# Performance work log

Measured on AMD Instinct MI355X. Metric: run time of the kernel, lower is better.

## Reference

```python
import jax, jax.numpy as jnp
import numpy as np

B, S, L, T = 32, 512, 20, 16
E, H, D = 300, 128, 128
V = 50000
SEG = S // T


def _gru_dir(x, Wi, Wh, bi, bh, reverse):
    """One direction of torch-style GRU. x: (B,S,E). Returns (outs (B,S,H), h_final (B,H))."""
    xs = jnp.swapaxes(x, 0, 1)  # (S,B,E)
    h0 = jnp.zeros((x.shape[0], H), x.dtype)

    def step(h, x_t):
        gi = x_t @ Wi.T + bi          # (B,3H) gates order: r,z,n (torch)
        gh = h @ Wh.T + bh
        r = jax.nn.sigmoid(gi[:, :H] + gh[:, :H])
        z = jax.nn.sigmoid(gi[:, H:2 * H] + gh[:, H:2 * H])
        n = jnp.tanh(gi[:, 2 * H:] + r * gh[:, 2 * H:])
        h_new = (1.0 - z) * n + z * h
        return h_new, h_new

    hN, hs = jax.lax.scan(step, h0, xs, reverse=reverse)
    return jnp.swapaxes(hs, 0, 1), hN


def setup_inputs() -> dict:
    key = jax.random.key(0)
    ks = jax.random.split(key, 16)
    word_ids = jax.random.randint(ks[0], (B, S, L), 0, V, dtype=jnp.int32)
    # contiguous, full-coverage topic segments, 1-based boundaries (as in the torch code)
    starts = jnp.tile(jnp.arange(T, dtype=jnp.int32) * SEG + 1, (B, 1))
    ends = jnp.tile((jnp.arange(T, dtype=jnp.int32) + 1) * SEG, (B, 1))
    sent2topic = jnp.tile((jnp.arange(S, dtype=jnp.int32) // SEG), (B, 1))
    sc = 0.08
    return {
        "word_ids": word_ids, "starts": starts, "ends": ends, "sent2topic": sent2topic,
        "embed_table": jax.random.normal(ks[1], (V, E), jnp.float32) * 0.6,
        "Wi_f": jax.random.normal(ks[2], (3 * H, E), jnp.float32) * sc,
        "Wh_f": jax.random.normal(ks[3], (3 * H, H), jnp.float32) * sc,
        "bi_f": jax.random.normal(ks[4], (3 * H,), jnp.float32) * sc,
        "bh_f": jax.random.normal(ks[5], (3 * H,), jnp.float32) * sc,
        "Wi_b": jax.random.normal(ks[6], (3 * H, E), jnp.float32) * sc,
        "Wh_b": jax.random.normal(ks[7], (3 * H, H), jnp.float32) * sc,
        "bi_b": jax.random.normal(ks[8], (3 * H,), jnp.float32) * sc,
        "bh_b": jax.random.normal(ks[9], (3 * H,), jnp.float32) * sc,
        "W_att": jax.random.normal(ks[10], (4 * H, 4 * H), jnp.float32) * 0.05,
        "v_att": jax.random.normal(ks[11], (4 * H, 1), jnp.float32) * 0.05,
        "W1": jax.random.normal(ks[12], (D, 4 * H), jnp.float32) * 0.05,
        "b1": jax.random.normal(ks[13], (D,), jnp.float32) * 0.05,
        "W2": jax.random.normal(ks[14], (1, D), jnp.float32) * 0.05,
        "b2": jax.random.normal(ks[15], (1,), jnp.float32) * 0.05,
    }


def reference(word_ids, starts, ends, sent2topic, embed_table,
              Wi_f, Wh_f, bi_f, bh_f, Wi_b, Wh_b, bi_b, bh_b,
              W_att, v_att, W1, b1, W2, b2):
    # --- sent_encoder: mean of word embeddings per sentence ---
    sent = jnp.take(embed_table, word_ids, axis=0).mean(axis=2)  # (B,S,E)
    # --- doc_encoder: bidirectional GRU ---
    out_f, h_f = _gru_dir(sent, Wi_f, Wh_f, bi_f, bh_f, reverse=False)
    out_b, h_b = _gru_dir(sent, Wi_b, Wh_b, bi_b, bh_b, reverse=True)
    sent_rep = jnp.concatenate([out_f, out_b], axis=-1)          # (B,S,2H)
    # faithful to torch: hidden (2,B,H).view(B,2H)
    hidden = jnp.stack([h_f, h_b], axis=0)
    doc_rep = hidden.reshape(B, 2 * H)
    doc_rep = jnp.broadcast_to(doc_rep[None], (S, B, 2 * H)).swapaxes(0, 1)  # (B,S,2H)
    # --- topic_rep: boundary diffs (padded index i == 1-based sentence i) ---
    padded = jnp.pad(sent_rep, ((0, 0), (1, 1), (0, 0)))          # (B,S+2,2H)
    g = lambda idx: jnp.take_along_axis(padded, idx[:, :, None], axis=1)  # (B,T,2H)
    fwd_diff = g(ends)[..., :H] - g(starts - 1)[..., :H]
    bwd_diff = g(starts)[..., H:] - g(ends + 1)[..., H:]
    topic_mat = jnp.concatenate([fwd_diff, bwd_diff], axis=-1)   # (B,T,2H)
    topic_rep = jnp.take_along_axis(topic_mat, sent2topic[:, :, None], axis=1)  # (B,S,2H)
    # --- decoder ---
    cat_ds = jnp.concatenate([doc_rep, sent_rep], axis=-1)       # (B,S,4H)
    cat_ts = jnp.concatenate([topic_rep, sent_rep], axis=-1)
    doc_scores = jnp.tanh(cat_ds @ W_att) @ v_att                # (B,S,1)
    topic_scores = jnp.tanh(cat_ts @ W_att) @ v_att
    sum_scores = doc_scores + topic_scores
    doc_w = doc_scores / sum_scores
    topic_w = topic_scores / sum_scores
    context = doc_w * doc_rep + topic_w * topic_rep
    inp = jnp.concatenate([sent_rep, context], axis=-1)          # (B,S,4H)
    h = jax.nn.relu(inp @ W1.T + b1)                             # dropout=eval identity
    logits = (h @ W2.T + b2).squeeze(-1)                         # (B,S)
    return logits
```

## Files before the change

kernel.cpp:

```cpp
#include <hip/hip_runtime.h>


#define LDS_BARRIER() do {                                   \
    asm volatile("s_waitcnt lgkmcnt(0)" ::: "memory");       \
    __builtin_amdgcn_s_barrier();                            \
    asm volatile("" ::: "memory");                           \
  } while (0)

__global__ __launch_bounds__(128) void k_sent_mean(
    const int* __restrict__ wid, const float* __restrict__ emb,
    float* __restrict__ sent)
{
  const int bs = blockIdx.x;
  const int tid = threadIdx.x;
  const int* w = wid + (size_t)bs * 20;
  float a0 = 0.f, a1 = 0.f, a2 = 0.f;
  for (int l = 0; l < 20; ++l) {
    const float* row = emb + (size_t)w[l] * 300;
    a0 += row[tid];
    a1 += row[tid + 128];
    if (tid < 44) a2 += row[tid + 256];
  }
  const float inv = 1.0f / 20.0f;
  float* o = sent + (size_t)bs * 300;
  o[tid] = a0 * inv;
  o[tid + 128] = a1 * inv;
  if (tid < 44) o[tid + 256] = a2 * inv;
}

template<bool BT, int ACT>
__global__ __launch_bounds__(256) void k_gemm(
    const int M, const int N, const int K,
    const float* __restrict__ A, const int lda,
    const float* __restrict__ Bm, const int ldb,
    float* __restrict__ C, const int ldc,
    const float* __restrict__ bias)
{
  (void)N;
  __shared__ float As[64][68];
  __shared__ float Bs[64][68];
  const int tid = threadIdx.x;
  const int m0 = blockIdx.x * 64;
  const int n0 = blockIdx.y * 64;
  const int tx = tid & 15;
  const int ty = tid >> 4;
  float acc[4][4] = {};

  for (int kc = 0; kc < K; kc += 64) {
    const int kb = (K - kc < 64) ? (K - kc) : 64;
    #pragma unroll
    for (int r = 0; r < 4; ++r) {
      const int m = r * 16 + ty;
      const int k4 = tx * 4;
      float4 v = make_float4(0.f, 0.f, 0.f, 0.f);
      if (m0 + m < M) {
        const float* ap = A + (size_t)(m0 + m) * lda + kc;
        if (k4 + 4 <= kb) {
          v = *(const float4*)(ap + k4);
        } else {
          float t0 = (k4 + 0 < kb) ? ap[k4 + 0] : 0.f;
          float t1 = (k4 + 1 < kb) ? ap[k4 + 1] : 0.f;
          float t2 = (k4 + 2 < kb) ? ap[k4 + 2] : 0.f;
          float t3 = (k4 + 3 < kb) ? ap[k4 + 3] : 0.f;
          v = make_float4(t0, t1, t2, t3);
        }
      }
      *(float4*)&As[m][k4] = v;
    }
    if (BT) {
      #pragma unroll
      for (int r = 0; r < 4; ++r) {
        const int n = r * 16 + ty;
        const int k4 = tx * 4;
        float4 v = make_float4(0.f, 0.f, 0.f, 0.f);
        const float* bp = Bm + (size_t)(n0 + n) * ldb + kc;
        if (k4 + 4 <= kb) {
          v = *(const float4*)(bp + k4);
        } else {
          float t0 = (k4 + 0 < kb) ? bp[k4 + 0] : 0.f;
          float t1 = (k4 + 1 < kb) ? bp[k4 + 1] : 0.f;
          float t2 = (k4 + 2 < kb) ? bp[k4 + 2] : 0.f;
          float t3 = (k4 + 3 < kb) ? bp[k4 + 3] : 0.f;
          v = make_float4(t0, t1, t2, t3);
        }
        Bs[k4 + 0][n] = v.x;
        Bs[k4 + 1][n] = v.y;
        Bs[k4 + 2][n] = v.z;
        Bs[k4 + 3][n] = v.w;
      }
    } else {
      #pragma unroll
      for (int r = 0; r < 4; ++r) {
        const int kk = r * 16 + ty;
        const int n4 = tx * 4;
        float4 v = make_float4(0.f, 0.f, 0.f, 0.f);
        if (kk < kb) v = *(const float4*)(Bm + (size_t)(kc + kk) * ldb + n0 + n4);
        *(float4*)&Bs[kk][n4] = v;
      }
    }
    __syncthreads();
    #pragma unroll 4
    for (int kk = 0; kk < kb; ++kk) {
      const float4 bv = *(const float4*)&Bs[kk][tx * 4];
      #pragma unroll
      for (int i = 0; i < 4; ++i) {
        const float a = As[ty * 4 + i][kk];
        acc[i][0] = fmaf(a, bv.x, acc[i][0]);
        acc[i][1] = fmaf(a, bv.y, acc[i][1]);
        acc[i][2] = fmaf(a, bv.z, acc[i][2]);
        acc[i][3] = fmaf(a, bv.w, acc[i][3]);
      }
    }
    __syncthreads();
  }

  float bv4[4] = {0.f, 0.f, 0.f, 0.f};
  if (bias != nullptr) {
    #pragma unroll
    for (int j = 0; j < 4; ++j) bv4[j] = bias[n0 + tx * 4 + j];
  }
  #pragma unroll
  for (int i = 0; i < 4; ++i) {
    const int m = m0 + ty * 4 + i;
    if (m < M) {
      float4 o;
      o.x = acc[i][0] + bv4[0];
      o.y = acc[i][1] + bv4[1];
      o.z = acc[i][2] + bv4[2];
      o.w = acc[i][3] + bv4[3];
      if (ACT == 1) {
        o.x = fmaxf(o.x, 0.f); o.y = fmaxf(o.y, 0.f);
        o.z = fmaxf(o.z, 0.f); o.w = fmaxf(o.w, 0.f);
      }
      *(float4*)&C[(size_t)m * ldc + n0 + tx * 4] = o;
    }
  }
}

__global__ __launch_bounds__(512, 2) void k_gru(
    const float* __restrict__ gi_f, const float* __restrict__ gi_b,
    const float* __restrict__ Wh_f, const float* __restrict__ Wh_b,
    const float* __restrict__ bh_f, const float* __restrict__ bh_b,
    float* __restrict__ srep, float* __restrict__ hfin)
{
  const int dir = blockIdx.x & 1;
  const int b = blockIdx.x >> 1;
  const float* gi = (dir ? gi_b : gi_f) + (size_t)b * 512 * 384;
  const float* Wh = dir ? Wh_b : Wh_f;
  const float* bh = dir ? bh_b : bh_f;

  const int tid = threadIdx.x;
  const int wv = tid >> 6;
  const int ln = tid & 63;
  const int kq = wv & 3;
  const int rg = wv >> 2;
  const int r0 = rg * 192 + ln;

  __shared__ __align__(16) float hlds[128];
  __shared__ float partl[4 * 384];
  __shared__ __align__(16) float gis[2][32 * 384];

  float4 w0[8], w1[8], w2[8];
  {
    const float* p = Wh + (size_t)r0 * 128 + kq * 32;
    #pragma unroll
    for (int kk = 0; kk < 8; ++kk) w0[kk] = *(const float4*)(p + kk * 4);
    p += 64 * 128;
    #pragma unroll
    for (int kk = 0; kk < 8; ++kk) w1[kk] = *(const float4*)(p + kk * 4);
    p += 64 * 128;
    #pragma unroll
    for (int kk = 0; kk < 8; ++kk) w2[kk] = *(const float4*)(p + kk * 4);
  }
  const float bh0 = (kq == 0) ? bh[r0] : 0.f;
  const float bh1 = (kq == 0) ? bh[r0 + 64] : 0.f;
  const float bh2 = (kq == 0) ? bh[r0 + 128] : 0.f;

  {
    const int lo0 = dir ? 480 : 0;
    const float4* g4 = (const float4*)(gi + (size_t)lo0 * 384);
    float4* l4 = (float4*)gis[0];
    #pragma unroll
    for (int j = 0; j < 6; ++j) l4[j * 512 + tid] = g4[j * 512 + tid];
  }
  float hreg = 0.f;
  if (tid < 128) hlds[tid] = 0.f;
  LDS_BARRIER();

  const float4* h4q = (const float4*)hlds + kq * 8;
  float4 stg[6];

  for (int c = 0; c < 16; ++c) {
    const int buf = c & 1;
    const int lo = dir ? (480 - 32 * c) : (32 * c);
    if (c < 15) {
      const int lon = dir ? (480 - 32 * (c + 1)) : (32 * (c + 1));
      const float4* g4 = (const float4*)(gi + (size_t)lon * 384);
      #pragma unroll
      for (int j = 0; j < 6; ++j) stg[j] = g4[j * 512 + tid];
    }

    for (int i = 0; i < 32; ++i) {
      const int sloc = dir ? (31 - i) : i;
      const int seq = lo + sloc;

      float4 A0 = {0.f, 0.f, 0.f, 0.f};
      float4 A1 = {0.f, 0.f, 0.f, 0.f};
      float4 A2 = {0.f, 0.f, 0.f, 0.f};
      #pragma unroll
      for (int kk = 0; kk < 8; ++kk) {
        const float4 hv = h4q[kk];
        A0.x = fmaf(w0[kk].x, hv.x, A0.x);
        A0.y = fmaf(w0[kk].y, hv.y, A0.y);
        A0.z = fmaf(w0[kk].z, hv.z, A0.z);
        A0.w = fmaf(w0[kk].w, hv.w, A0.w);
        A1.x = fmaf(w1[kk].x, hv.x, A1.x);
        A1.y = fmaf(w1[kk].y, hv.y, A1.y);
        A1.z = fmaf(w1[kk].z, hv.z, A1.z);
        A1.w = fmaf(w1[kk].w, hv.w, A1.w);
        A2.x = fmaf(w2[kk].x, hv.x, A2.x);
        A2.y = fmaf(w2[kk].y, hv.y, A2.y);
        A2.z = fmaf(w2[kk].z, hv.z, A2.z);
        A2.w = fmaf(w2[kk].w, hv.w, A2.w);
      }
      partl[kq * 384 + r0]       = (A0.x + A0.y) + (A0.z + A0.w) + bh0;
      partl[kq * 384 + r0 + 64]  = (A1.x + A1.y) + (A1.z + A1.w) + bh1;
      partl[kq * 384 + r0 + 128] = (A2.x + A2.y) + (A2.z + A2.w) + bh2;
      LDS_BARRIER();

      if (tid < 128) {
        const float* grow = &gis[buf][sloc * 384];
        const float ghr = (partl[tid]       + partl[384 + tid])
                        + (partl[768 + tid] + partl[1152 + tid]);
        const float ghz = (partl[tid + 128]        + partl[384 + tid + 128])
                        + (partl[768 + tid + 128]  + partl[1152 + tid + 128]);
        const float ghn = (partl[tid + 256]        + partl[384 + tid + 256])
                        + (partl[768 + tid + 256]  + partl[1152 + tid + 256]);
        const float gir = grow[tid];
        const float giz = grow[tid + 128];
        const float gin = grow[tid + 256];
        const float r = __fdividef(1.f, 1.f + __expf(-(gir + ghr)));
        const float z = __fdividef(1.f, 1.f + __expf(-(giz + ghz)));
        float an = gin + r * ghn;
        an = fminf(fmaxf(an, -15.f), 15.f);
        const float t = __expf(2.f * an);
        const float n = __fdividef(t - 1.f, t + 1.f);
        hreg = (1.f - z) * n + z * hreg;
        hlds[tid] = hreg;
        srep[((size_t)(b * 512 + seq)) * 256 + dir * 128 + tid] = hreg;
      }
      LDS_BARRIER();
    }

    if (c < 15) {
      float4* l4 = (float4*)gis[buf ^ 1];
      #pragma unroll
      for (int j = 0; j < 6; ++j) l4[j * 512 + tid] = stg[j];
      LDS_BARRIER();
    }
  }
  if (tid < 128) hfin[(size_t)dir * 4096 + (size_t)b * 128 + tid] = hreg;
}

__global__ __launch_bounds__(256) void k_topic(
    const int* __restrict__ starts, const int* __restrict__ ends,
    const float* __restrict__ srep, float* __restrict__ tmat)
{
  const int bt = blockIdx.x;
  const int b = bt >> 4;
  const int st = starts[bt], en = ends[bt];
  const int j = threadIdx.x;
  float v;
  if (j < 128) {
    const float a = (en >= 1 && en <= 512) ? srep[((size_t)(b * 512 + en - 1)) * 256 + j] : 0.f;
    const float c = (st - 1 >= 1 && st - 1 <= 512) ? srep[((size_t)(b * 512 + st - 2)) * 256 + j] : 0.f;
    v = a - c;
  } else {
    const float a = (st >= 1 && st <= 512) ? srep[((size_t)(b * 512 + st - 1)) * 256 + j] : 0.f;
    const float c = (en + 1 >= 1 && en + 1 <= 512) ? srep[((size_t)(b * 512 + en)) * 256 + j] : 0.f;
    v = a - c;
  }
  tmat[(size_t)bt * 256 + j] = v;
}

__global__ __launch_bounds__(256) void k_scores(
    const float* spart, const float* __restrict__ docp, const float* __restrict__ topp,
    const float* __restrict__ v_att, const float* __restrict__ srep,
    const float* __restrict__ docrep, const float* __restrict__ tmat,
    const int* __restrict__ s2t, float* inp)
{
  const int bs = blockIdx.x;
  const int b = bs >> 9;
  const int tid = threadIdx.x;
  const int tp = s2t[bs];
  const float* sp = spart + (size_t)bs * 512;
  const float* dp = docp + (size_t)b * 512;
  const float* tq = topp + ((size_t)(b * 16 + tp)) * 512;
  float ds = 0.f, ts = 0.f;
  #pragma unroll
  for (int r = 0; r < 2; ++r) {
    const int o = tid + r * 256;
    const float s0 = sp[o], v = v_att[o];
    ds += tanhf(s0 + dp[o]) * v;
    ts += tanhf(s0 + tq[o]) * v;
  }
  #pragma unroll
  for (int off = 32; off; off >>= 1) {
    ds += __shfl_down(ds, off);
    ts += __shfl_down(ts, off);
  }
  __shared__ float rds[4], rts[4], wsh[2];
  const int wv = tid >> 6, ln = tid & 63;
  if (ln == 0) { rds[wv] = ds; rts[wv] = ts; }
  __syncthreads();
  if (tid == 0) {
    const float D = rds[0] + rds[1] + rds[2] + rds[3];
    const float T = rts[0] + rts[1] + rts[2] + rts[3];
    const float sum = D + T;
    wsh[0] = D / sum;
    wsh[1] = T / sum;
  }
  __syncthreads();
  const float dw = wsh[0], tw = wsh[1];
  const float sr = srep[(size_t)bs * 256 + tid];
  const float ctx = dw * docrep[(size_t)b * 256 + tid]
                  + tw * tmat[((size_t)(b * 16 + tp)) * 256 + tid];
  float* op = inp + (size_t)bs * 512;
  op[tid] = sr;
  op[256 + tid] = ctx;
}

__global__ __launch_bounds__(64) void k_logits(
    const float* __restrict__ hbuf, const float* __restrict__ W2,
    const float* __restrict__ b2, float* __restrict__ out)
{
  const int bs = blockIdx.x;
  const int ln = threadIdx.x;
  const float* h = hbuf + (size_t)bs * 128;
  float a = fmaf(h[ln], W2[ln], h[ln + 64] * W2[ln + 64]);
  #pragma unroll
  for (int off = 32; off; off >>= 1) a += __shfl_down(a, off);
  if (ln == 0) out[bs] = a + b2[0];
}

extern "C" void kernel_launch(void* const* d_in, const int* in_sizes, int n_in,
                              void* d_out, int out_size, void* d_ws, size_t ws_size,
                              hipStream_t stream)
{
  (void)in_sizes; (void)n_in; (void)out_size;

  const int*   word_ids = (const int*)d_in[0];
  const int*   starts   = (const int*)d_in[1];
  const int*   ends     = (const int*)d_in[2];
  const int*   s2t      = (const int*)d_in[3];
  const float* emb      = (const float*)d_in[4];
  const float* Wi_f     = (const float*)d_in[5];
  const float* Wh_f     = (const float*)d_in[6];
  const float* bi_f     = (const float*)d_in[7];
  const float* bh_f     = (const float*)d_in[8];
  const float* Wi_b     = (const float*)d_in[9];
  const float* Wh_b     = (const float*)d_in[10];
  const float* bi_b     = (const float*)d_in[11];
  const float* bh_b     = (const float*)d_in[12];
  const float* W_att    = (const float*)d_in[13];
  const float* v_att    = (const float*)d_in[14];
  const float* W1       = (const float*)d_in[15];
  const float* b1       = (const float*)d_in[16];
  const float* W2       = (const float*)d_in[17];
  const float* b2       = (const float*)d_in[18];
  float* out = (float*)d_out;

  char* ws = (char*)d_ws;
  if (ws_size < 88440832u) return;
  float* sent  = (float*)(ws + 0);
  float* gi_f  = (float*)(ws + 19660800);
  float* gi_b  = (float*)(ws + 44826624);
  float* srep  = (float*)(ws + 69992448);
  float* hfin  = (float*)(ws + 86769664);
  float* tmat  = (float*)(ws + 86802432);
  float* docp  = (float*)(ws + 87326720);
  float* topp  = (float*)(ws + 87392256);
  float* spart = (float*)(ws + 19660800);
  float* hbuf  = (float*)(ws + 0);

  k_sent_mean<<<16384, 128, 0, stream>>>(word_ids, emb, sent);
  k_gemm<true, 0><<<dim3(256, 6), 256, 0, stream>>>(16384, 384, 300, sent, 300, Wi_f, 300, gi_f, 384, bi_f);
  k_gemm<true, 0><<<dim3(256, 6), 256, 0, stream>>>(16384, 384, 300, sent, 300, Wi_b, 300, gi_b, 384, bi_b);
  k_gru<<<64, 512, 0, stream>>>(gi_f, gi_b, Wh_f, Wh_b, bh_f, bh_b, srep, hfin);
  k_topic<<<512, 256, 0, stream>>>(starts, ends, srep, tmat);
  k_gemm<false, 0><<<dim3(256, 8), 256, 0, stream>>>(16384, 512, 256, srep, 256, W_att + 256 * 512, 512, spart, 512, nullptr);
  k_gemm<false, 0><<<dim3(1, 8),   256, 0, stream>>>(32,    512, 256, hfin, 256, W_att,            512, docp,  512, nullptr);
  k_gemm<false, 0><<<dim3(8, 8),   256, 0, stream>>>(512,   512, 256, tmat, 256, W_att,            512, topp,  512, nullptr);
  k_scores<<<16384, 256, 0, stream>>>(spart, docp, topp, v_att, srep, hfin, tmat, s2t, spart);
  k_gemm<true, 1><<<dim3(256, 2), 256, 0, stream>>>(16384, 128, 512, spart, 512, W1, 512, hbuf, 128, b1);
  k_logits<<<16384, 64, 0, stream>>>(hbuf, W2, b2, out);
}
```

Measured before the change: 714.2 us.

## Fuse forward/backward input GEMMs, transpose A tile in LDS, vectorize sentence mean

Result: no change. 710.8 us (-0.5%).

```diff
diff --git a/kernel.cpp b/kernel.cpp
--- a/kernel.cpp
+++ b/kernel.cpp
@@ -7,25 +7,33 @@
     asm volatile("" ::: "memory");                           \
   } while (0)
 
+__global__ __launch_bounds__(256) void k_wcat(
+    const float* __restrict__ wf, const float* __restrict__ wb,
+    const float* __restrict__ bf, const float* __restrict__ bb,
+    float* __restrict__ Wcat, float* __restrict__ bcat)
+{
+  const int idx = blockIdx.x * 256 + threadIdx.x;
+  Wcat[idx] = wf[idx];
+  Wcat[115200 + idx] = wb[idx];
+  if (idx < 384) { bcat[idx] = bf[idx]; bcat[384 + idx] = bb[idx]; }
+}
+
 __global__ __launch_bounds__(128) void k_sent_mean(
     const int* __restrict__ wid, const float* __restrict__ emb,
     float* __restrict__ sent)
 {
   const int bs = blockIdx.x;
-  const int tid = threadIdx.x;
+  const int t = threadIdx.x;
   const int* w = wid + (size_t)bs * 20;
-  float a0 = 0.f, a1 = 0.f, a2 = 0.f;
+  if (t >= 75) return;
+  float4 a = {0.f, 0.f, 0.f, 0.f};
   for (int l = 0; l < 20; ++l) {
-    const float* row = emb + (size_t)w[l] * 300;
-    a0 += row[tid];
-    a1 += row[tid + 128];
-    if (tid < 44) a2 += row[tid + 256];
+    const float4 v = *(const float4*)(emb + (size_t)w[l] * 300 + t * 4);
+    a.x += v.x; a.y += v.y; a.z += v.z; a.w += v.w;
   }
   const float inv = 1.0f / 20.0f;
-  float* o = sent + (size_t)bs * 300;
-  o[tid] = a0 * inv;
-  o[tid + 128] = a1 * inv;
-  if (tid < 44) o[tid + 256] = a2 * inv;
+  a.x *= inv; a.y *= inv; a.z *= inv; a.w *= inv;
+  *(float4*)(sent + (size_t)bs * 300 + t * 4) = a;
 }
 
 template<bool BT, int ACT>
@@ -37,7 +45,7 @@
     const float* __restrict__ bias)
 {
   (void)N;
-  __shared__ float As[64][68];
+  __shared__ float Ast[64][68];
   __shared__ float Bs[64][68];
   const int tid = threadIdx.x;
   const int m0 = blockIdx.x * 64;
@@ -65,7 +73,10 @@
           v = make_float4(t0, t1, t2, t3);
         }
       }
-      *(float4*)&As[m][k4] = v;
+      Ast[k4 + 0][m] = v.x;
+      Ast[k4 + 1][m] = v.y;
+      Ast[k4 + 2][m] = v.z;
+      Ast[k4 + 3][m] = v.w;
     }
     if (BT) {
       #pragma unroll
@@ -101,15 +112,24 @@
     __syncthreads();
     #pragma unroll 4
     for (int kk = 0; kk < kb; ++kk) {
+      const float4 av = *(const float4*)&Ast[kk][ty * 4];
       const float4 bv = *(const float4*)&Bs[kk][tx * 4];
-      #pragma unroll
-      for (int i = 0; i < 4; ++i) {
-        const float a = As[ty * 4 + i][kk];
-        acc[i][0] = fmaf(a, bv.x, acc[i][0]);
-        acc[i][1] = fmaf(a, bv.y, acc[i][1]);
-        acc[i][2] = fmaf(a, bv.z, acc[i][2]);
-        acc[i][3] = fmaf(a, bv.w, acc[i][3]);
-      }
+      acc[0][0] = fmaf(av.x, bv.x, acc[0][0]);
+      acc[0][1] = fmaf(av.x, bv.y, acc[0][1]);
+      acc[0][2] = fmaf(av.x, bv.z, acc[0][2]);
+      acc[0][3] = fmaf(av.x, bv.w, acc[0][3]);
+      acc[1][0] = fmaf(av.y, bv.x, acc[1][0]);
+      acc[1][1] = fmaf(av.y, bv.y, acc[1][1]);
+      acc[1][2] = fmaf(av.y, bv.z, acc[1][2]);
+      acc[1][3] = fmaf(av.y, bv.w, acc[1][3]);
+      acc[2][0] = fmaf(av.z, bv.x, acc[2][0]);
+      acc[2][1] = fmaf(av.z, bv.y, acc[2][1]);
+      acc[2][2] = fmaf(av.z, bv.z, acc[2][2]);
+      acc[2][3] = fmaf(av.z, bv.w, acc[2][3]);
+      acc[3][0] = fmaf(av.w, bv.x, acc[3][0]);
+      acc[3][1] = fmaf(av.w, bv.y, acc[3][1]);
+      acc[3][2] = fmaf(av.w, bv.z, acc[3][2]);
+      acc[3][3] = fmaf(av.w, bv.w, acc[3][3]);
     }
     __syncthreads();
   }
@@ -138,14 +158,14 @@
 }
 
 __global__ __launch_bounds__(512, 2) void k_gru(
-    const float* __restrict__ gi_f, const float* __restrict__ gi_b,
+    const float* __restrict__ gi_fb,
     const float* __restrict__ Wh_f, const float* __restrict__ Wh_b,
     const float* __restrict__ bh_f, const float* __restrict__ bh_b,
     float* __restrict__ srep, float* __restrict__ hfin)
 {
   const int dir = blockIdx.x & 1;
   const int b = blockIdx.x >> 1;
-  const float* gi = (dir ? gi_b : gi_f) + (size_t)b * 512 * 384;
+  const float* gi = gi_fb + (size_t)b * 512 * 768 + dir * 384;
   const float* Wh = dir ? Wh_b : Wh_f;
   const float* bh = dir ? bh_b : bh_f;
 
@@ -178,10 +198,15 @@
 
   {
     const int lo0 = dir ? 480 : 0;
-    const float4* g4 = (const float4*)(gi + (size_t)lo0 * 384);
+    const float4* g4 = (const float4*)(gi + (size_t)lo0 * 768);
     float4* l4 = (float4*)gis[0];
     #pragma unroll
-    for (int j = 0; j < 6; ++j) l4[j * 512 + tid] = g4[j * 512 + tid];
+    for (int j = 0; j < 6; ++j) {
+      const int f = j * 512 + tid;
+      const int row = f / 96;
+      const int col = f - row * 96;
+      l4[f] = g4[row * 192 + col];
+    }
   }
   float hreg = 0.f;
   if (tid < 128) hlds[tid] = 0.f;
@@ -195,9 +220,14 @@
     const int lo = dir ? (480 - 32 * c) : (32 * c);
     if (c < 15) {
       const int lon = dir ? (480 - 32 * (c + 1)) : (32 * (c + 1));
-      const float4* g4 = (const float4*)(gi + (size_t)lon * 384);
+      const float4* g4 = (const float4*)(gi + (size_t)lon * 768);
       #pragma unroll
-      for (int j = 0; j < 6; ++j) stg[j] = g4[j * 512 + tid];
+      for (int j = 0; j < 6; ++j) {
+        const int f = j * 512 + tid;
+        const int row = f / 96;
+        const int col = f - row * 96;
+        stg[j] = g4[row * 192 + col];
+      }
     }
 
     for (int i = 0; i < 32; ++i) {
@@ -373,8 +403,7 @@
   char* ws = (char*)d_ws;
   if (ws_size < 88440832u) return;
   float* sent  = (float*)(ws + 0);
-  float* gi_f  = (float*)(ws + 19660800);
-  float* gi_b  = (float*)(ws + 44826624);
+  float* gi_fb = (float*)(ws + 19660800);
   float* srep  = (float*)(ws + 69992448);
   float* hfin  = (float*)(ws + 86769664);
   float* tmat  = (float*)(ws + 86802432);
@@ -382,11 +411,13 @@
   float* topp  = (float*)(ws + 87392256);
   float* spart = (float*)(ws + 19660800);
   float* hbuf  = (float*)(ws + 0);
+  float* Wcat  = (float*)(ws + 69992448);
+  float* bcat  = (float*)(ws + 70914048);
 
   k_sent_mean<<<16384, 128, 0, stream>>>(word_ids, emb, sent);
-  k_gemm<true, 0><<<dim3(256, 6), 256, 0, stream>>>(16384, 384, 300, sent, 300, Wi_f, 300, gi_f, 384, bi_f);
-  k_gemm<true, 0><<<dim3(256, 6), 256, 0, stream>>>(16384, 384, 300, sent, 300, Wi_b, 300, gi_b, 384, bi_b);
-  k_gru<<<64, 512, 0, stream>>>(gi_f, gi_b, Wh_f, Wh_b, bh_f, bh_b, srep, hfin);
+  k_wcat<<<450, 256, 0, stream>>>(Wi_f, Wi_b, bi_f, bi_b, Wcat, bcat);
+  k_gemm<true, 0><<<dim3(256, 12), 256, 0, stream>>>(16384, 768, 300, sent, 300, Wcat, 300, gi_fb, 768, bcat);
+  k_gru<<<64, 512, 0, stream>>>(gi_fb, Wh_f, Wh_b, bh_f, bh_b, srep, hfin);
   k_topic<<<512, 256, 0, stream>>>(starts, ends, srep, tmat);
   k_gemm<false, 0><<<dim3(256, 8), 256, 0, stream>>>(16384, 512, 256, srep, 256, W_att + 256 * 512, 512, spart, 512, nullptr);
   k_gemm<false, 0><<<dim3(1, 8),   256, 0, stream>>>(32,    512, 256, hfin, 256, W_att,            512, docp,  512, nullptr);
```
